# Performance work log

Hardware: AMD Instinct MI355X
Metric: run time of the kernel (lower is better)

## Reference

```python
import math
import jax, jax.numpy as jnp
import numpy as np

B, T, C, H = 2, 2048, 1024, 16
HD = C // H
ALPHA = 32.0


def setup_inputs() -> dict:
    key = jax.random.key(0)
    ks = jax.random.split(key, 16)
    s = 0.02
    inp = {
        "query": jax.random.normal(ks[0], (B, T, C), jnp.float32),
        "key": jax.random.normal(ks[1], (B, T, C), jnp.float32),
        "value": jax.random.normal(ks[2], (B, T, C), jnp.float32),
        # causal mask: 0 => masked (matches masked_fill(att_mask == 0, -inf))
        "att_mask": jnp.tril(jnp.ones((1, 1, T, T), jnp.float32)),
        "Wq": jax.random.normal(ks[3], (C, C), jnp.float32) * s,
        "bq": jnp.zeros((C,), jnp.float32),
        "Wk": jax.random.normal(ks[4], (C, C), jnp.float32) * s,
        "bk": jnp.zeros((C,), jnp.float32),
        "Wv": jax.random.normal(ks[5], (C, C), jnp.float32) * s,
        "bv": jnp.zeros((C,), jnp.float32),
        "Wp": jax.random.normal(ks[6], (C, C), jnp.float32) * s,
        "bp": jnp.zeros((C,), jnp.float32),
    }
    return inp


def reference(query, key, value, att_mask, Wq, bq, Wk, bk, Wv, bv, Wp, bp):
    b, tq, c = query.shape
    tk = key.shape[1]
    # separate QKV projections, split heads: [B,H,T,HD]
    q = (query @ Wq + bq).reshape(b, tq, H, HD).transpose(0, 2, 1, 3)
    k = (key @ Wk + bk).reshape(b, tk, H, HD).transpose(0, 2, 1, 3)
    v = (value @ Wv + bv).reshape(b, tk, H, HD).transpose(0, 2, 1, 3)
    # PBrelax: pre-scale q by 1/(alpha*sqrt(hd)), subtract detached global abs-max, rescale
    att = jnp.einsum("bhqd,bhkd->bhqk", q * (1.0 / ALPHA / math.sqrt(HD)), k)
    att = (att - jax.lax.stop_gradient(jnp.max(jnp.abs(att)))) * ALPHA
    att = jnp.where(att_mask[:, :, :tq, :tk] == 0, -jnp.inf, att)
    att = jax.nn.softmax(att, axis=-1)
    y = jnp.einsum("bhqk,bhkd->bhqd", att, v)
    y = y.transpose(0, 2, 1, 3).reshape(b, tq, c)
    return y @ Wp + bp
```

## Files before the change

### kernel.cpp

```cpp
#include <hip/hip_runtime.h>


#define Bsz 2
#define Tsz 2048
#define Csz 1024
#define Hsz 16
#define HDsz 64

typedef __bf16 bf16;
typedef __bf16 bf16x8 __attribute__((ext_vector_type(8)));
typedef __bf16 bf16x4 __attribute__((ext_vector_type(4)));
typedef float float4v __attribute__((ext_vector_type(4)));

#define MFMA16(a, b, c) __builtin_amdgcn_mfma_f32_16x16x32_bf16(a, b, c, 0, 0, 0)

#define GLOAD_LDS16(gptr, lptr)                                      \
  __builtin_amdgcn_global_load_lds(                                  \
      (const __attribute__((address_space(1))) void*)(gptr),         \
      (__attribute__((address_space(3))) void*)(lptr), 16, 0, 0)

__global__ __launch_bounds__(256) void cast3_bf16(
    const float* __restrict__ q, const float* __restrict__ k,
    const float* __restrict__ v, bf16* __restrict__ oq,
    bf16* __restrict__ ok, bf16* __restrict__ ov) {
  const int z = blockIdx.z;
  const float* src = z == 0 ? q : (z == 1 ? k : v);
  bf16* dst = z == 0 ? oq : (z == 1 ? ok : ov);
  const size_t i = ((size_t)blockIdx.x * 256 + threadIdx.x) * 8;
  const float4 a = *(const float4*)(src + i);
  const float4 b = *(const float4*)(src + i + 4);
  bf16x8 o;
  o[0] = (bf16)a.x; o[1] = (bf16)a.y; o[2] = (bf16)a.z; o[3] = (bf16)a.w;
  o[4] = (bf16)b.x; o[5] = (bf16)b.y; o[6] = (bf16)b.z; o[7] = (bf16)b.w;
  *(bf16x8*)(dst + i) = o;
}

__global__ __launch_bounds__(256) void wtrans_bf16(
    const float* __restrict__ Wq, const float* __restrict__ Wk,
    const float* __restrict__ Wv, const float* __restrict__ Wp,
    bf16* __restrict__ WT) {
  const int z = blockIdx.z;
  const float* W = z == 0 ? Wq : (z == 1 ? Wk : (z == 2 ? Wv : Wp));
  bf16* out = WT + (size_t)z * (Csz * Csz);
  __shared__ float Ts[64][68];
  const int k0 = blockIdx.y * 64, n0 = blockIdx.x * 64;
  const int tid = threadIdx.x;
#pragma unroll
  for (int it = 0; it < 4; ++it) {
    const int idx = it * 256 + tid;
    const int r = idx >> 4, c4 = (idx & 15) * 4;
    *(float4*)&Ts[r][c4] = *(const float4*)(W + (size_t)(k0 + r) * Csz + n0 + c4);
  }
  __syncthreads();
#pragma unroll
  for (int it = 0; it < 2; ++it) {
    const int idx = it * 256 + tid;
    const int n = idx & 63, k8 = (idx >> 6) * 8;
    bf16x8 o;
#pragma unroll
    for (int j = 0; j < 8; ++j) o[j] = (bf16)Ts[k8 + j][n];
    *(bf16x8*)(out + (size_t)(n0 + n) * Csz + k0 + k8) = o;
  }
}

__global__ __launch_bounds__(512, 2) void gemm256_qkv(
    const bf16* __restrict__ A0, const bf16* __restrict__ A1,
    const bf16* __restrict__ A2, const bf16* __restrict__ Wt,
    const float* __restrict__ b0, const float* __restrict__ b1,
    const float* __restrict__ b2, bf16* __restrict__ C0,
    bf16* __restrict__ C1, bf16* __restrict__ Vt) {
  constexpr int NT = Csz / 64;
  const int z = blockIdx.z;
  const bf16* A = z == 0 ? A0 : (z == 1 ? A1 : A2);
  const float* bias = z == 0 ? b0 : (z == 1 ? b1 : b2);
  const bf16* Bt = Wt + (size_t)z * (Csz * Csz);
  const int m0 = blockIdx.y * 256;
  const int nz0 = blockIdx.x * 256;

  __shared__ bf16 As[2 * 256 * 64];
  __shared__ bf16 Bs[2 * 256 * 64];

  const int tid = threadIdx.x;
  const int wave = tid >> 6, lane = tid & 63;
  const int l15 = lane & 15, quad = lane >> 4;
  const int wm = wave >> 2, wn = wave & 3;

  const int srow = tid >> 3;
  const int sch = tid & 7;
  const bf16* Ab = A + (size_t)(m0 + srow) * Csz + (sch ^ (srow & 7)) * 8;
  const bf16* Bb = Bt + (size_t)(nz0 + srow) * Csz + (sch ^ (srow & 7)) * 8;

#define STG(Xb, lds, lbuf, hh, tt)                                           \
  {                                                                          \
    GLOAD_LDS16((Xb) + (size_t)((hh)*128) * Csz + (size_t)(tt)*64,           \
                &(lds)[(lbuf) * (256 * 64) + (hh)*8192 + tid * 8]);          \
    GLOAD_LDS16((Xb) + (size_t)((hh)*128 + 64) * Csz + (size_t)(tt)*64,     \
                &(lds)[(lbuf) * (256 * 64) + (hh)*8192 + 4096 + tid * 8]);  \
  }
#define RD_A(dst, lbuf, i2, ks)                                              \
  dst = *(const bf16x8*)&As[(lbuf) * (256 * 64) +                            \
                            (wm * 128 + (i2)*16 + l15) * 64 +                \
                            ((((ks)*4 + quad) ^ (l15 & 7)) * 8)];
#define RD_B(dst, lbuf, j2, ks)                                              \
  dst = *(const bf16x8*)&Bs[(lbuf) * (256 * 64) +                            \
                            (wn * 64 + (j2)*16 + l15) * 64 +                 \
                            ((((ks)*4 + quad) ^ (l15 & 7)) * 8)];

  float4v acc[8][4];
#pragma unroll
  for (int i = 0; i < 8; ++i)
#pragma unroll
    for (int j = 0; j < 4; ++j) acc[i][j] = (float4v){0.f, 0.f, 0.f, 0.f};

  STG(Ab, As, 0, 0, 0);
  STG(Ab, As, 0, 1, 0);
  STG(Bb, Bs, 0, 0, 0);
  STG(Bb, Bs, 0, 1, 0);
  STG(Ab, As, 1, 0, 1);
  STG(Ab, As, 1, 1, 1);
  asm volatile("s_waitcnt vmcnt(4)" ::: "memory");
  __builtin_amdgcn_s_barrier();
  __builtin_amdgcn_sched_barrier(0);

#pragma unroll 1
  for (int t = 0; t < NT; ++t) {
    const int bsel = t & 1;
    bf16x8 af0[4][2], af1[4][2], bf0[2][2], bf1[2][2];

#pragma unroll
    for (int i = 0; i < 4; ++i) {
      RD_A(af0[i][0], bsel, i, 0);
      RD_A(af0[i][1], bsel, i, 1);
    }
#pragma unroll
    for (int j = 0; j < 2; ++j) {
      RD_B(bf0[j][0], bsel, j, 0);
      RD_B(bf0[j][1], bsel, j, 1);
    }
    if (t + 1 < NT) STG(Bb, Bs, bsel ^ 1, 0, t + 1);
    __builtin_amdgcn_s_barrier();
    asm volatile("s_waitcnt lgkmcnt(0)" ::: "memory");
    __builtin_amdgcn_sched_barrier(0);
    __builtin_amdgcn_s_setprio(1);
#pragma unroll
    for (int i = 0; i < 4; ++i)
#pragma unroll
      for (int j = 0; j < 2; ++j) {
        acc[i][j] = MFMA16(af0[i][0], bf0[j][0], acc[i][j]);
        acc[i][j] = MFMA16(af0[i][1], bf0[j][1], acc[i][j]);
      }
    __builtin_amdgcn_s_setprio(0);
    __builtin_amdgcn_s_barrier();

#pragma unroll
    for (int i = 0; i < 4; ++i) {
      RD_A(af1[i][0], bsel, 4 + i, 0);
      RD_A(af1[i][1], bsel, 4 + i, 1);
    }
    if (t + 1 < NT) STG(Bb, Bs, bsel ^ 1, 1, t + 1);
    __builtin_amdgcn_s_barrier();
    asm volatile("s_waitcnt lgkmcnt(0)" ::: "memory");
    __builtin_amdgcn_sched_barrier(0);
    __builtin_amdgcn_s_setprio(1);
#pragma unroll
    for (int i = 0; i < 4; ++i)
#pragma unroll
      for (int j = 0; j < 2; ++j) {
        acc[4 + i][j] = MFMA16(af1[i][0], bf0[j][0], acc[4 + i][j]);
        acc[4 + i][j] = MFMA16(af1[i][1], bf0[j][1], acc[4 + i][j]);
      }
    __builtin_amdgcn_s_setprio(0);
    __builtin_amdgcn_s_barrier();

#pragma unroll
    for (int j = 0; j < 2; ++j) {
      RD_B(bf1[j][0], bsel, 2 + j, 0);
      RD_B(bf1[j][1], bsel, 2 + j, 1);
    }
    if (t + 2 < NT) STG(Ab, As, bsel, 0, t + 2);
    __builtin_amdgcn_s_barrier();
    asm volatile("s_waitcnt lgkmcnt(0)" ::: "memory");
    __builtin_amdgcn_sched_barrier(0);
    __builtin_amdgcn_s_setprio(1);
#pragma unroll
    for (int i = 0; i < 4; ++i)
#pragma unroll
      for (int j = 0; j < 2; ++j) {
        acc[i][2 + j] = MFMA16(af0[i][0], bf1[j][0], acc[i][2 + j]);
        acc[i][2 + j] = MFMA16(af0[i][1], bf1[j][1], acc[i][2 + j]);
      }
    __builtin_amdgcn_s_setprio(0);
    __builtin_amdgcn_s_barrier();

    if (t + 2 < NT) STG(Ab, As, bsel, 1, t + 2);
    __builtin_amdgcn_s_barrier();
    __builtin_amdgcn_s_setprio(1);
#pragma unroll
    for (int i = 0; i < 4; ++i)
#pragma unroll
      for (int j = 0; j < 2; ++j) {
        acc[4 + i][2 + j] = MFMA16(af1[i][0], bf1[j][0], acc[4 + i][2 + j]);
        acc[4 + i][2 + j] = MFMA16(af1[i][1], bf1[j][1], acc[4 + i][2 + j]);
      }
    __builtin_amdgcn_s_setprio(0);
    if (t + 2 < NT) {
      asm volatile("s_waitcnt vmcnt(4)" ::: "memory");
    } else if (t + 1 < NT) {
      asm volatile("s_waitcnt vmcnt(0)" ::: "memory");
    }
    __builtin_amdgcn_s_barrier();
    __builtin_amdgcn_sched_barrier(0);
  }
#undef STG
#undef RD_A
#undef RD_B

  const int omb0 = m0 + wm * 128 + quad * 4;
  const int onb0 = nz0 + wn * 64 + l15;
  if (z == 2) {
#pragma unroll
    for (int j = 0; j < 4; ++j) {
      const int n = onb0 + j * 16;
      const float bj = bias[n];
#pragma unroll
      for (int i = 0; i < 8; ++i) {
        const int mrow = omb0 + i * 16;
        const int bb = mrow >> 11, tt = mrow & (Tsz - 1);
        union { bf16 h[4]; uint2 u; } pk;
#pragma unroll
        for (int r = 0; r < 4; ++r) pk.h[r] = (bf16)(acc[i][j][r] + bj);
        *(uint2*)(Vt + ((size_t)(bb * 1024 + n)) * Tsz + tt) = pk.u;
      }
    }
  } else {
    bf16* C = z == 0 ? C0 : C1;
    const float osc = z == 0 ? 0.180336880111124f : 1.0f;
#pragma unroll
    for (int j = 0; j < 4; ++j) {
      const float bj = bias[onb0 + j * 16];
#pragma unroll
      for (int i = 0; i < 8; ++i) {
#pragma unroll
        for (int r = 0; r < 4; ++r) {
          const float v = (acc[i][j][r] + bj) * osc;
          C[(size_t)(omb0 + i * 16 + r) * Csz + onb0 + j * 16] = (bf16)v;
        }
      }
    }
  }
}

template <typename OutT, bool VTR>
__global__ __launch_bounds__(256) void gemm_mfma(
    const bf16* __restrict__ A0, const bf16* __restrict__ A1,
    const bf16* __restrict__ A2, const bf16* __restrict__ Wt,
    const float* __restrict__ b0, const float* __restrict__ b1,
    const float* __restrict__ b2, OutT* __restrict__ C0,
    OutT* __restrict__ C1, OutT* __restrict__ C2, int M, int N, int K) {
  const int z = blockIdx.z;
  const bf16* A = z == 0 ? A0 : (z == 1 ? A1 : A2);
  const float* bias = z == 0 ? b0 : (z == 1 ? b1 : b2);
  OutT* C = z == 0 ? C0 : (z == 1 ? C1 : C2);
  const bf16* Bt = Wt + (size_t)z * N * K;
  const float osc = (VTR && z == 0) ? 0.180336880111124f : 1.0f;

  __shared__ bf16 As[128 * 32];
  __shared__ bf16 Bs[128 * 32];
  const int tid = threadIdx.x;
  const int wave = tid >> 6, lane = tid & 63;
  const int l15 = lane & 15, quad = lane >> 4;
  const int m0 = blockIdx.y * 128, n0 = blockIdx.x * 128;
  const int wm = (wave >> 1) * 64, wn = (wave & 1) * 64;
  const int srow = tid >> 2, schunk = tid & 3;

  float4v acc[4][4];
#pragma unroll
  for (int i = 0; i < 4; ++i)
#pragma unroll
    for (int j = 0; j < 4; ++j) acc[i][j] = (float4v){0.f, 0.f, 0.f, 0.f};

  for (int k0 = 0; k0 < K; k0 += 32) {
    __syncthreads();
#pragma unroll
    for (int p = 0; p < 2; ++p) {
      const int row = p * 64 + srow;
      GLOAD_LDS16(A + (size_t)(m0 + row) * K + k0 + schunk * 8,
                  &As[(p * 256 + tid) * 8]);
      GLOAD_LDS16(Bt + (size_t)(n0 + row) * K + k0 + schunk * 8,
                  &Bs[(p * 256 + tid) * 8]);
    }
    __syncthreads();

    bf16x8 af[4], bfr[4];
#pragma unroll
    for (int i = 0; i < 4; ++i)
      af[i] = *(const bf16x8*)&As[(wm + i * 16 + l15) * 32 + quad * 8];
#pragma unroll
    for (int j = 0; j < 4; ++j)
      bfr[j] = *(const bf16x8*)&Bs[(wn + j * 16 + l15) * 32 + quad * 8];
#pragma unroll
    for (int i = 0; i < 4; ++i)
#pragma unroll
      for (int j = 0; j < 4; ++j)
        acc[i][j] = MFMA16(af[i], bfr[j], acc[i][j]);
  }

  const int omb = m0 + wm + quad * 4;
  const int onb = n0 + wn + l15;
  if (VTR && z == 2) {
#pragma unroll
    for (int j = 0; j < 4; ++j) {
      const int n = onb + j * 16;
      const float bj = bias[n];
#pragma unroll
      for (int i = 0; i < 4; ++i) {
        const int mrow = omb + i * 16;
        const int bb = mrow >> 11, t = mrow & (Tsz - 1);
        union { bf16 h[4]; uint2 u; } pk;
#pragma unroll
        for (int r = 0; r < 4; ++r) pk.h[r] = (bf16)(acc[i][j][r] + bj);
        *(uint2*)((bf16*)C + ((size_t)(bb * 1024 + n)) * Tsz + t) = pk.u;
      }
    }
  } else {
#pragma unroll
    for (int j = 0; j < 4; ++j) {
      const float bj = bias[onb + j * 16];
#pragma unroll
      for (int i = 0; i < 4; ++i) {
#pragma unroll
        for (int r = 0; r < 4; ++r) {
          const float v = (acc[i][j][r] + bj) * osc;
          const size_t off = (size_t)(omb + i * 16 + r) * N + onb + j * 16;
          if constexpr (sizeof(OutT) == 2)
            C[off] = (OutT)v;
          else
            C[off] = v;
        }
      }
    }
  }
}

__global__ __launch_bounds__(256) void attn_mfma(const bf16* __restrict__ Q,
                                                 const bf16* __restrict__ K,
                                                 const bf16* __restrict__ Vt,
                                                 bf16* __restrict__ Y) {
  __shared__ bf16 Ks[2][64 * 64];
  __shared__ bf16 Vs[2][64 * 64];
  __shared__ bf16 Ps[4][32 * 72];

  const int bh = blockIdx.y;
  const int b = bh >> 4, h = bh & 15;
  int xr = (blockIdx.x & 1) ? (int)(gridDim.x - 1 - (blockIdx.x >> 1))
                            : (int)(blockIdx.x >> 1);
  if (bh >= 16) xr = (int)(gridDim.x - 1) - xr;
  const int i0 = xr * 128;
  const int tid = threadIdx.x;
  const int wave = tid >> 6, lane = tid & 63;
  const int l15 = lane & 15, quad = lane >> 4;

  const int srow = tid >> 3;
  const int sch = tid & 7;

  const bf16* kb = K + (size_t)b * Tsz * Csz + h * HDsz;
  const bf16* vb = Vt + (size_t)bh * HDsz * Tsz;

  const int qb = i0 + wave * 32;

  bf16x8 qf[2][2];
#pragma unroll
  for (int sub = 0; sub < 2; ++sub) {
    const bf16* qp =
        Q + ((size_t)(b * Tsz + qb + sub * 16 + l15)) * Csz + h * HDsz + quad * 8;
    qf[sub][0] = *(const bf16x8*)qp;
    qf[sub][1] = *(const bf16x8*)(qp + 32);
  }

  bf16x8 ones;
#pragma unroll
  for (int j = 0; j < 8; ++j) ones[j] = (bf16)1.0f;

  float4v Of[2][4];
  float4v accl[2];
#pragma unroll
  for (int sub = 0; sub < 2; ++sub) {
    accl[sub] = (float4v){0.f, 0.f, 0.f, 0.f};
#pragma unroll
    for (int nc = 0; nc < 4; ++nc) Of[sub][nc] = (float4v){0.f, 0.f, 0.f, 0.f};
  }

  const int ntile = i0 / 64 + 2;

#define STAGE_KV(tt, bb)                                                     \
  {                                                                          \
    _Pragma("unroll") for (int p = 0; p < 2; ++p) {                          \
      const int r = p * 32 + srow;                                           \
      const int c = sch ^ (r & 7);                                           \
      GLOAD_LDS16(kb + (size_t)((tt)*64 + r) * Csz + c * 8,                  \
                  &Ks[bb][(p * 256 + tid) * 8]);                             \
      GLOAD_LDS16(vb + (size_t)r * Tsz + (tt)*64 + c * 8,                    \
                  &Vs[bb][(p * 256 + tid) * 8]);                             \
    }                                                                        \
  }

  STAGE_KV(0, 0);
  asm volatile("s_waitcnt vmcnt(0)" ::: "memory");
  __builtin_amdgcn_s_barrier();
  __builtin_amdgcn_sched_barrier(0);

#pragma unroll 1
  for (int t = 0; t < ntile; ++t) {
    const int j0 = t * 64;
    const int buf = t & 1;
    if (t + 1 < ntile) STAGE_KV(t + 1, buf ^ 1);

    if (j0 <= qb + 31) {
      float4v S[2][4];
#pragma unroll
      for (int nc = 0; nc < 4; ++nc) {
        const int row = nc * 16 + l15;
        const bf16x8 k0 =
            *(const bf16x8*)&Ks[buf][row * 64 + ((quad ^ (row & 7)) * 8)];
        const bf16x8 k1 =
            *(const bf16x8*)&Ks[buf][row * 64 + (((quad + 4) ^ (row & 7)) * 8)];
#pragma unroll
        for (int sub = 0; sub < 2; ++sub) {
          float4v a = (float4v){0.f, 0.f, 0.f, 0.f};
          a = MFMA16(k0, qf[sub][0], a);
          a = MFMA16(k1, qf[sub][1], a);
          S[sub][nc] = a;
        }
      }

      if (j0 + 63 > qb) {
#pragma unroll
        for (int sub = 0; sub < 2; ++sub) {
          const int q = qb + sub * 16 + l15;
#pragma unroll
          for (int nc = 0; nc < 4; ++nc) {
            const int keyb = j0 + nc * 16 + quad * 4;
#pragma unroll
            for (int r = 0; r < 4; ++r)
              if (keyb + r > q) S[sub][nc][r] = -1e30f;
          }
        }
      }

#pragma unroll
      for (int sub = 0; sub < 2; ++sub) {
#pragma unroll
        for (int nc = 0; nc < 4; ++nc) {
          bf16x4 pk;
#pragma unroll
          for (int r = 0; r < 4; ++r)
            pk[r] = (bf16)__builtin_amdgcn_exp2f(S[sub][nc][r]);
          *(bf16x4*)&Ps[wave][(sub * 16 + l15) * 72 + nc * 16 + quad * 4] = pk;
        }
      }

      bf16x8 pf[2][2];
#pragma unroll
      for (int sub = 0; sub < 2; ++sub) {
#pragma unroll
        for (int kc = 0; kc < 2; ++kc)
          pf[sub][kc] = *(const bf16x8*)
              &Ps[wave][(sub * 16 + l15) * 72 + kc * 32 + quad * 8];
        accl[sub] = MFMA16(ones, pf[sub][0], accl[sub]);
        accl[sub] = MFMA16(ones, pf[sub][1], accl[sub]);
      }
#pragma unroll
      for (int nc = 0; nc < 4; ++nc) {
        const int row = nc * 16 + l15;
#pragma unroll
        for (int kc = 0; kc < 2; ++kc) {
          const bf16x8 vf = *(const bf16x8*)
              &Vs[buf][row * 64 + (((kc * 4 + quad) ^ (row & 7)) * 8)];
#pragma unroll
          for (int sub = 0; sub < 2; ++sub)
            Of[sub][nc] = MFMA16(vf, pf[sub][kc], Of[sub][nc]);
        }
      }
    }

    if (t + 1 < ntile) {
      asm volatile("s_waitcnt vmcnt(0)" ::: "memory");
    }
    __builtin_amdgcn_sched_barrier(0);
    __builtin_amdgcn_s_barrier();
    __builtin_amdgcn_sched_barrier(0);
  }
#undef STAGE_KV

#pragma unroll
  for (int sub = 0; sub < 2; ++sub) {
    const float rl = __builtin_amdgcn_rcpf(accl[sub][0]);
    const size_t rowoff =
        ((size_t)(b * Tsz + qb + sub * 16 + l15)) * Csz + h * HDsz;
#pragma unroll
    for (int nc = 0; nc < 4; ++nc) {
      union { bf16 h4[4]; uint2 u; } pk;
#pragma unroll
      for (int r = 0; r < 4; ++r) pk.h4[r] = (bf16)(Of[sub][nc][r] * rl);
      *(uint2*)(Y + rowoff + nc * 16 + quad * 4) = pk.u;
    }
  }
}

extern "C" void kernel_launch(void* const* d_in, const int* in_sizes, int n_in,
                              void* d_out, int out_size, void* d_ws,
                              size_t ws_size, hipStream_t stream) {
  const float* query = (const float*)d_in[0];
  const float* key = (const float*)d_in[1];
  const float* value = (const float*)d_in[2];
  const float* Wq = (const float*)d_in[4];
  const float* bq = (const float*)d_in[5];
  const float* Wk = (const float*)d_in[6];
  const float* bk = (const float*)d_in[7];
  const float* Wv = (const float*)d_in[8];
  const float* bv = (const float*)d_in[9];
  const float* Wp = (const float*)d_in[10];
  const float* bp = (const float*)d_in[11];
  float* out = (float*)d_out;

  char* ws = (char*)d_ws;
  bf16* WT = (bf16*)(ws);
  bf16* vc = (bf16*)(ws + (8u << 20));
  bf16* Qp = (bf16*)(ws + (16u << 20));
  bf16* Kp = (bf16*)(ws + (24u << 20));
  bf16* Vt = (bf16*)(ws + (32u << 20));
  bf16* Yb = vc;
  bf16* qc = (bf16*)d_out;
  bf16* kc = (bf16*)((char*)d_out + (8u << 20));

  const int M = Bsz * Tsz;

  cast3_bf16<<<dim3((M * Csz) / (256 * 8), 1, 3), dim3(256), 0, stream>>>(
      query, key, value, qc, kc, vc);
  wtrans_bf16<<<dim3(16, 16, 4), dim3(256), 0, stream>>>(Wq, Wk, Wv, Wp, WT);
  gemm256_qkv<<<dim3(Csz / 256, M / 256, 3), dim3(512), 0, stream>>>(
      qc, kc, vc, WT, bq, bk, bv, Qp, Kp, Vt);
  attn_mfma<<<dim3(Tsz / 128, Bsz * Hsz), dim3(256), 0, stream>>>(Qp, Kp, Vt,
                                                                  Yb);
  gemm_mfma<float, false><<<dim3(Csz / 128, M / 128, 1), dim3(256), 0, stream>>>(
      Yb, Yb, Yb, WT + 3u * (Csz * Csz), bp, bp, bp, out, out, out, M, Csz,
      Csz);
}
```

Measured before the change: 246.5 us.

## Shrink output-projection GEMM tile and rotate attention KV tile order

The output projection GEMM becomes a dedicated kernel with 128x64 tiles instead of 128x128. That doubles the grid to 512 blocks and should fill the CUs better, at the cost of more A-matrix reloads. The attention kernel drops the zig-zag block remapping and uses a direct block index. Half of the blocks, picked by parity, start their KV loop in the middle of the range and wrap around. This is meant to spread concurrent K/V reads across different tiles and reduce contention. The per-block work imbalance of causal attention is now left to the hardware scheduler.

After: 251.0 us. About the same (+1.8%).

```diff
diff --git a/kernel.cpp b/kernel.cpp
--- a/kernel.cpp
+++ b/kernel.cpp
@@ -250,94 +250,61 @@
   }
 }
 
-template <typename OutT, bool VTR>
-__global__ __launch_bounds__(256) void gemm_mfma(
-    const bf16* __restrict__ A0, const bf16* __restrict__ A1,
-    const bf16* __restrict__ A2, const bf16* __restrict__ Wt,
-    const float* __restrict__ b0, const float* __restrict__ b1,
-    const float* __restrict__ b2, OutT* __restrict__ C0,
-    OutT* __restrict__ C1, OutT* __restrict__ C2, int M, int N, int K) {
-  const int z = blockIdx.z;
-  const bf16* A = z == 0 ? A0 : (z == 1 ? A1 : A2);
-  const float* bias = z == 0 ? b0 : (z == 1 ? b1 : b2);
-  OutT* C = z == 0 ? C0 : (z == 1 ? C1 : C2);
-  const bf16* Bt = Wt + (size_t)z * N * K;
-  const float osc = (VTR && z == 0) ? 0.180336880111124f : 1.0f;
-
+__global__ __launch_bounds__(256) void gemm_op(
+    const bf16* __restrict__ A, const bf16* __restrict__ Bt,
+    const float* __restrict__ bias, float* __restrict__ C) {
   __shared__ bf16 As[128 * 32];
-  __shared__ bf16 Bs[128 * 32];
+  __shared__ bf16 Bs[64 * 32];
   const int tid = threadIdx.x;
   const int wave = tid >> 6, lane = tid & 63;
   const int l15 = lane & 15, quad = lane >> 4;
-  const int m0 = blockIdx.y * 128, n0 = blockIdx.x * 128;
-  const int wm = (wave >> 1) * 64, wn = (wave & 1) * 64;
+  const int m0 = blockIdx.y * 128, n0 = blockIdx.x * 64;
+  const int wm = (wave >> 1) * 64, wn = (wave & 1) * 32;
   const int srow = tid >> 2, schunk = tid & 3;
 
-  float4v acc[4][4];
+  float4v acc[4][2];
 #pragma unroll
   for (int i = 0; i < 4; ++i)
 #pragma unroll
-    for (int j = 0; j < 4; ++j) acc[i][j] = (float4v){0.f, 0.f, 0.f, 0.f};
-
-  for (int k0 = 0; k0 < K; k0 += 32) {
+    for (int j = 0; j < 2; ++j) acc[i][j] = (float4v){0.f, 0.f, 0.f, 0.f};
+
+  for (int k0 = 0; k0 < Csz; k0 += 32) {
     __syncthreads();
 #pragma unroll
     for (int p = 0; p < 2; ++p) {
       const int row = p * 64 + srow;
-      GLOAD_LDS16(A + (size_t)(m0 + row) * K + k0 + schunk * 8,
+      GLOAD_LDS16(A + (size_t)(m0 + row) * Csz + k0 + schunk * 8,
                   &As[(p * 256 + tid) * 8]);
-      GLOAD_LDS16(Bt + (size_t)(n0 + row) * K + k0 + schunk * 8,
-                  &Bs[(p * 256 + tid) * 8]);
-    }
+    }
+    GLOAD_LDS16(Bt + (size_t)(n0 + srow) * Csz + k0 + schunk * 8,
+                &Bs[tid * 8]);
     __syncthreads();
 
-    bf16x8 af[4], bfr[4];
+    bf16x8 af[4], bfr[2];
 #pragma unroll
     for (int i = 0; i < 4; ++i)
       af[i] = *(const bf16x8*)&As[(wm + i * 16 + l15) * 32 + quad * 8];
 #pragma unroll
-    for (int j = 0; j < 4; ++j)
+    for (int j = 0; j < 2; ++j)
       bfr[j] = *(const bf16x8*)&Bs[(wn + j * 16 + l15) * 32 + quad * 8];
 #pragma unroll
     for (int i = 0; i < 4; ++i)
 #pragma unroll
-      for (int j = 0; j < 4; ++j)
+      for (int j = 0; j < 2; ++j)
         acc[i][j] = MFMA16(af[i], bfr[j], acc[i][j]);
   }
 
   const int omb = m0 + wm + quad * 4;
   const int onb = n0 + wn + l15;
-  if (VTR && z == 2) {
-#pragma unroll
-    for (int j = 0; j < 4; ++j) {
-      const int n = onb + j * 16;
-      const float bj = bias[n];
-#pragma unroll
-      for (int i = 0; i < 4; ++i) {
-        const int mrow = omb + i * 16;
-        const int bb = mrow >> 11, t = mrow & (Tsz - 1);
-        union { bf16 h[4]; uint2 u; } pk;
-#pragma unroll
-        for (int r = 0; r < 4; ++r) pk.h[r] = (bf16)(acc[i][j][r] + bj);
-        *(uint2*)((bf16*)C + ((size_t)(bb * 1024 + n)) * Tsz + t) = pk.u;
-      }
-    }
-  } else {
-#pragma unroll
-    for (int j = 0; j < 4; ++j) {
-      const float bj = bias[onb + j * 16];
-#pragma unroll
-      for (int i = 0; i < 4; ++i) {
-#pragma unroll
-        for (int r = 0; r < 4; ++r) {
-          const float v = (acc[i][j][r] + bj) * osc;
-          const size_t off = (size_t)(omb + i * 16 + r) * N + onb + j * 16;
-          if constexpr (sizeof(OutT) == 2)
-            C[off] = (OutT)v;
-          else
-            C[off] = v;
-        }
-      }
+#pragma unroll
+  for (int j = 0; j < 2; ++j) {
+    const float bj = bias[onb + j * 16];
+#pragma unroll
+    for (int i = 0; i < 4; ++i) {
+#pragma unroll
+      for (int r = 0; r < 4; ++r)
+        C[(size_t)(omb + i * 16 + r) * Csz + onb + j * 16] =
+            acc[i][j][r] + bj;
     }
   }
 }
@@ -352,9 +319,7 @@
 
   const int bh = blockIdx.y;
   const int b = bh >> 4, h = bh & 15;
-  int xr = (blockIdx.x & 1) ? (int)(gridDim.x - 1 - (blockIdx.x >> 1))
-                            : (int)(blockIdx.x >> 1);
-  if (bh >= 16) xr = (int)(gridDim.x - 1) - xr;
+  const int xr = (int)blockIdx.x;
   const int i0 = xr * 128;
   const int tid = threadIdx.x;
   const int wave = tid >> 6, lane = tid & 63;
@@ -391,6 +356,7 @@
   }
 
   const int ntile = i0 / 64 + 2;
+  const int s0 = ((xr ^ (bh >> 4)) & 1) ? (ntile >> 1) : 0;
 
 #define STAGE_KV(tt, bb)                                                     \
   {                                                                          \
@@ -404,16 +370,22 @@
     }                                                                        \
   }
 
-  STAGE_KV(0, 0);
+  STAGE_KV(s0, 0);
   asm volatile("s_waitcnt vmcnt(0)" ::: "memory");
   __builtin_amdgcn_s_barrier();
   __builtin_amdgcn_sched_barrier(0);
 
 #pragma unroll 1
-  for (int t = 0; t < ntile; ++t) {
-    const int j0 = t * 64;
-    const int buf = t & 1;
-    if (t + 1 < ntile) STAGE_KV(t + 1, buf ^ 1);
+  for (int s = 0; s < ntile; ++s) {
+    int tp = s + s0;
+    if (tp >= ntile) tp -= ntile;
+    const int j0 = tp * 64;
+    const int buf = s & 1;
+    if (s + 1 < ntile) {
+      int tn = tp + 1;
+      if (tn >= ntile) tn -= ntile;
+      STAGE_KV(tn, buf ^ 1);
+    }
 
     if (j0 <= qb + 31) {
       float4v S[2][4];
@@ -483,7 +455,7 @@
       }
     }
 
-    if (t + 1 < ntile) {
+    if (s + 1 < ntile) {
       asm volatile("s_waitcnt vmcnt(0)" ::: "memory");
     }
     __builtin_amdgcn_sched_barrier(0);
@@ -542,7 +514,6 @@
       qc, kc, vc, WT, bq, bk, bv, Qp, Kp, Vt);
   attn_mfma<<<dim3(Tsz / 128, Bsz * Hsz), dim3(256), 0, stream>>>(Qp, Kp, Vt,
                                                                   Yb);
-  gemm_mfma<float, false><<<dim3(Csz / 128, M / 128, 1), dim3(256), 0, stream>>>(
-      Yb, Yb, Yb, WT + 3u * (Csz * Csz), bp, bp, bp, out, out, out, M, Csz,
-      Csz);
+  gemm_op<<<dim3(Csz / 64, M / 128), dim3(256), 0, stream>>>(
+      Yb, WT + 3u * (Csz * Csz), bp, out);
 }
```
